# Kernel tuning notes

Measured on AMD Instinct MI355X. Metric: run time of the kernel, lower is better.

## Reference

```python
import jax, jax.numpy as jnp
import numpy as np

B, H = 65536, 512


def setup_inputs() -> dict:
    key = jax.random.key(0)
    ks = jax.random.split(key, 10)
    s = 1.0 / np.sqrt(H)  # torch nn.Linear default init range
    uni = lambda k, shape: jax.random.uniform(k, shape, jnp.float32, -s, s)
    return {
        "inputs": jax.random.normal(ks[0], (B, H), jnp.float32),
        "short_term_memory": jax.random.normal(ks[1], (B, H), jnp.float32),
        "Wf": uni(ks[2], (H, H)), "bf": uni(ks[3], (H,)),
        "Wi": uni(ks[4], (H, H)), "bi": uni(ks[5], (H,)),
        "Wg": uni(ks[6], (H, H)), "bg": uni(ks[7], (H,)),
        "Wo": uni(ks[8], (H, H)), "bo": uni(ks[9], (H,)),
    }


def reference(inputs, short_term_memory, Wf, bf, Wi, bi, Wg, bg, Wo, bo):
    z = inputs + short_term_memory  # [B, H]
    # ForgetGate: OVERWRITES long-term memory (previous cell state never read).
    c = jax.nn.sigmoid(z @ Wf.T + bf)
    # InputGate: c += sigmoid(...) * tanh(...)
    c = c + jax.nn.sigmoid(z @ Wi.T + bi) * jnp.tanh(z @ Wg.T + bg)
    # OutputGate: h = tanh(c) * sigmoid(...)
    h = jnp.tanh(c) * jax.nn.sigmoid(z @ Wo.T + bo)
    return jnp.stack((c, h))  # [2, B, H]: new long-term and short-term memory
```

## Files before the change

### kernel.cpp

```cpp
#include <hip/hip_runtime.h>

typedef __bf16 bf16x8 __attribute__((ext_vector_type(8)));
typedef float  f32x4  __attribute__((ext_vector_type(4)));

#define LOG2E 1.4426950408889634f

static __device__ __forceinline__ float fexp2(float x) { return __builtin_amdgcn_exp2f(x); }
static __device__ __forceinline__ float frcp(float x)  { return __builtin_amdgcn_rcpf(x); }
static __device__ __forceinline__ float fsigmoid(float x) { return frcp(1.0f + fexp2(-LOG2E * x)); }
static __device__ __forceinline__ float ftanh(float x)    { return 2.0f * frcp(1.0f + fexp2(-2.0f * LOG2E * x)) - 1.0f; }

__global__ __launch_bounds__(256) void wpack(const float* __restrict__ Wf,
                                             const float* __restrict__ Wi,
                                             const float* __restrict__ Wg,
                                             const float* __restrict__ Wo,
                                             __bf16* __restrict__ Wp)
{
    int idx = blockIdx.x * 256 + threadIdx.x;
    int kg  = idx & 63;
    int j   = (idx >> 6) & 511;
    int g   = idx >> 15;
    const float* src = (g == 0) ? Wf : (g == 1) ? Wi : (g == 2) ? Wg : Wo;
    const float4* s4 = (const float4*)(src + j * 512 + kg * 8);
    float4 v0 = s4[0], v1 = s4[1];
    bf16x8 o;
    o[0] = (__bf16)v0.x; o[1] = (__bf16)v0.y; o[2] = (__bf16)v0.z; o[3] = (__bf16)v0.w;
    o[4] = (__bf16)v1.x; o[5] = (__bf16)v1.y; o[6] = (__bf16)v1.z; o[7] = (__bf16)v1.w;
    int cn = j >> 4;
    int ks = kg >> 2;
    int lt = (j & 15) + (kg & 3) * 16;
    size_t dst = ((size_t)(((cn * 16 + ks) * 4 + g) * 64 + lt)) * 8;
    *(bf16x8*)(Wp + dst) = o;
}

__global__ __launch_bounds__(512, 2) void lstm_main(
    const float* __restrict__ xin, const float* __restrict__ stm,
    const __bf16* __restrict__ Wp,
    const float* __restrict__ bfv, const float* __restrict__ biv,
    const float* __restrict__ bgv, const float* __restrict__ bov,
    float* __restrict__ out)
{
    __shared__ unsigned char zs[131072];
    const int tid  = threadIdx.x;
    const int lane = tid & 63;
    const int wv   = tid >> 6;
    const int l15  = lane & 15;
    const int lq   = lane >> 4;
    const int row0 = blockIdx.x * 128;

    {
        const float* xb = xin + (size_t)row0 * 512;
        const float* sb = stm + (size_t)row0 * 512;
        #pragma unroll
        for (int it = 0; it < 16; ++it) {
            int idx = it * 512 + tid;
            int row = idx >> 6;
            int kg  = idx & 63;
            const float4* x4 = (const float4*)(xb + row * 512 + kg * 8);
            const float4* s4 = (const float4*)(sb + row * 512 + kg * 8);
            float4 a0 = x4[0], a1 = x4[1];
            float4 b0 = s4[0], b1 = s4[1];
            bf16x8 p;
            p[0] = (__bf16)(a0.x + b0.x); p[1] = (__bf16)(a0.y + b0.y);
            p[2] = (__bf16)(a0.z + b0.z); p[3] = (__bf16)(a0.w + b0.w);
            p[4] = (__bf16)(a1.x + b1.x); p[5] = (__bf16)(a1.y + b1.y);
            p[6] = (__bf16)(a1.z + b1.z); p[7] = (__bf16)(a1.w + b1.w);
            int rb   = row >> 5;
            int kk   = kg >> 1;
            int slot = ((row & 31) + (kg & 1) * 32) ^ (kk & 7);
            *(bf16x8*)(zs + rb * 32768 + kk * 1024 + slot * 16) = p;
        }
    }
    __syncthreads();

    const int kkoff = lq >> 1;
    const int sl0   = l15 + (lq & 1) * 32;
    const int koffb = kkoff << 10;

#define LOADB(B0, B1, B2, B3, KS) { \
    const char* a_ = bp + (KS) * 4096; \
    asm volatile("global_load_dwordx4 %0, %4, off\n\t" \
                 "global_load_dwordx4 %1, %4, off offset:1024\n\t" \
                 "global_load_dwordx4 %2, %4, off offset:2048\n\t" \
                 "global_load_dwordx4 %3, %4, off offset:3072" \
                 : "=&v"(B0), "=&v"(B1), "=&v"(B2), "=&v"(B3) : "v"(a_)); }
#define WAITB4 { asm volatile("s_waitcnt vmcnt(4)"); __builtin_amdgcn_sched_barrier(0x107); }
#define WAITB0 { asm volatile("s_waitcnt vmcnt(0)"); __builtin_amdgcn_sched_barrier(0x107); }
#define DOMFMA(B0, B1, B2, B3, KS) { \
    const int kk7_ = ((2 * (KS)) & 7) | kkoff; \
    const int t0_  = ((sl0 ^ kk7_) << 4) + (KS) * 2048 + koffb; \
    { \
        bf16x8 a0_ = *(const bf16x8*)(zs + t0_); \
        bf16x8 a1_ = *(const bf16x8*)(zs + t0_ + 256); \
        bf16x8 a2_ = *(const bf16x8*)(zs + 32768 + t0_); \
        bf16x8 a3_ = *(const bf16x8*)(zs + 32768 + t0_ + 256); \
        __builtin_amdgcn_s_setprio(1); \
        acc[0][0] = __builtin_amdgcn_mfma_f32_16x16x32_bf16(a0_, B0, acc[0][0], 0, 0, 0); \
        acc[1][0] = __builtin_amdgcn_mfma_f32_16x16x32_bf16(a1_, B0, acc[1][0], 0, 0, 0); \
        acc[2][0] = __builtin_amdgcn_mfma_f32_16x16x32_bf16(a2_, B0, acc[2][0], 0, 0, 0); \
        acc[3][0] = __builtin_amdgcn_mfma_f32_16x16x32_bf16(a3_, B0, acc[3][0], 0, 0, 0); \
        acc[0][1] = __builtin_amdgcn_mfma_f32_16x16x32_bf16(a0_, B1, acc[0][1], 0, 0, 0); \
        acc[1][1] = __builtin_amdgcn_mfma_f32_16x16x32_bf16(a1_, B1, acc[1][1], 0, 0, 0); \
        acc[2][1] = __builtin_amdgcn_mfma_f32_16x16x32_bf16(a2_, B1, acc[2][1], 0, 0, 0); \
        acc[3][1] = __builtin_amdgcn_mfma_f32_16x16x32_bf16(a3_, B1, acc[3][1], 0, 0, 0); \
        acc[0][2] = __builtin_amdgcn_mfma_f32_16x16x32_bf16(a0_, B2, acc[0][2], 0, 0, 0); \
        acc[1][2] = __builtin_amdgcn_mfma_f32_16x16x32_bf16(a1_, B2, acc[1][2], 0, 0, 0); \
        acc[2][2] = __builtin_amdgcn_mfma_f32_16x16x32_bf16(a2_, B2, acc[2][2], 0, 0, 0); \
        acc[3][2] = __builtin_amdgcn_mfma_f32_16x16x32_bf16(a3_, B2, acc[3][2], 0, 0, 0); \
        acc[0][3] = __builtin_amdgcn_mfma_f32_16x16x32_bf16(a0_, B3, acc[0][3], 0, 0, 0); \
        acc[1][3] = __builtin_amdgcn_mfma_f32_16x16x32_bf16(a1_, B3, acc[1][3], 0, 0, 0); \
        acc[2][3] = __builtin_amdgcn_mfma_f32_16x16x32_bf16(a2_, B3, acc[2][3], 0, 0, 0); \
        acc[3][3] = __builtin_amdgcn_mfma_f32_16x16x32_bf16(a3_, B3, acc[3][3], 0, 0, 0); \
        __builtin_amdgcn_s_setprio(0); \
    } \
    { \
        bf16x8 a4_ = *(const bf16x8*)(zs + 65536 + t0_); \
        bf16x8 a5_ = *(const bf16x8*)(zs + 65536 + t0_ + 256); \
        bf16x8 a6_ = *(const bf16x8*)(zs + 98304 + t0_); \
        bf16x8 a7_ = *(const bf16x8*)(zs + 98304 + t0_ + 256); \
        __builtin_amdgcn_s_setprio(1); \
        acc[4][0] = __builtin_amdgcn_mfma_f32_16x16x32_bf16(a4_, B0, acc[4][0], 0, 0, 0); \
        acc[5][0] = __builtin_amdgcn_mfma_f32_16x16x32_bf16(a5_, B0, acc[5][0], 0, 0, 0); \
        acc[6][0] = __builtin_amdgcn_mfma_f32_16x16x32_bf16(a6_, B0, acc[6][0], 0, 0, 0); \
        acc[7][0] = __builtin_amdgcn_mfma_f32_16x16x32_bf16(a7_, B0, acc[7][0], 0, 0, 0); \
        acc[4][1] = __builtin_amdgcn_mfma_f32_16x16x32_bf16(a4_, B1, acc[4][1], 0, 0, 0); \
        acc[5][1] = __builtin_amdgcn_mfma_f32_16x16x32_bf16(a5_, B1, acc[5][1], 0, 0, 0); \
        acc[6][1] = __builtin_amdgcn_mfma_f32_16x16x32_bf16(a6_, B1, acc[6][1], 0, 0, 0); \
        acc[7][1] = __builtin_amdgcn_mfma_f32_16x16x32_bf16(a7_, B1, acc[7][1], 0, 0, 0); \
        acc[4][2] = __builtin_amdgcn_mfma_f32_16x16x32_bf16(a4_, B2, acc[4][2], 0, 0, 0); \
        acc[5][2] = __builtin_amdgcn_mfma_f32_16x16x32_bf16(a5_, B2, acc[5][2], 0, 0, 0); \
        acc[6][2] = __builtin_amdgcn_mfma_f32_16x16x32_bf16(a6_, B2, acc[6][2], 0, 0, 0); \
        acc[7][2] = __builtin_amdgcn_mfma_f32_16x16x32_bf16(a7_, B2, acc[7][2], 0, 0, 0); \
        acc[4][3] = __builtin_amdgcn_mfma_f32_16x16x32_bf16(a4_, B3, acc[4][3], 0, 0, 0); \
        acc[5][3] = __builtin_amdgcn_mfma_f32_16x16x32_bf16(a5_, B3, acc[5][3], 0, 0, 0); \
        acc[6][3] = __builtin_amdgcn_mfma_f32_16x16x32_bf16(a6_, B3, acc[6][3], 0, 0, 0); \
        acc[7][3] = __builtin_amdgcn_mfma_f32_16x16x32_bf16(a7_, B3, acc[7][3], 0, 0, 0); \
        __builtin_amdgcn_s_setprio(0); \
    } }

    for (int ci = 0; ci < 4; ++ci) {
        const int cn   = ci * 8 + wv;
        const int colj = cn * 16 + l15;
        const char* bp = (const char*)Wp + (size_t)cn * 65536 + (size_t)lane * 16;

        float bias0 = bfv[colj], bias1 = biv[colj];
        float bias2 = bgv[colj], bias3 = bov[colj];
        f32x4 acc[8][4];
        #pragma unroll
        for (int m = 0; m < 8; ++m) {
            #pragma unroll
            for (int r = 0; r < 4; ++r) {
                acc[m][0][r] = bias0; acc[m][1][r] = bias1;
                acc[m][2][r] = bias2; acc[m][3][r] = bias3;
            }
        }

        bf16x8 P0, P1, P2, P3;
        bf16x8 Q0, Q1, Q2, Q3;

        asm volatile("s_waitcnt vmcnt(0)");
        __builtin_amdgcn_sched_barrier(0);
        LOADB(P0, P1, P2, P3, 0)
        #pragma unroll
        for (int ks = 0; ks < 16; ++ks) {
            if (ks < 15) {
                if ((ks + 1) & 1) { LOADB(Q0, Q1, Q2, Q3, ks + 1) }
                else              { LOADB(P0, P1, P2, P3, ks + 1) }
                WAITB4
            } else {
                WAITB0
            }
            if (ks & 1) { DOMFMA(Q0, Q1, Q2, Q3, ks) }
            else        { DOMFMA(P0, P1, P2, P3, ks) }
        }

        #pragma unroll
        for (int m = 0; m < 8; ++m) {
            #pragma unroll
            for (int r = 0; r < 4; ++r) {
                float F = acc[m][0][r], I = acc[m][1][r];
                float G = acc[m][2][r], O = acc[m][3][r];
                float c = fsigmoid(F) + fsigmoid(I) * ftanh(G);
                float h = ftanh(c) * fsigmoid(O);
                int row = row0 + m * 16 + lq * 4 + r;
                int o   = row * 512 + colj;
                out[o] = c;
                out[33554432 + o] = h;
            }
        }
    }
#undef LOADB
#undef WAITB4
#undef WAITB0
#undef DOMFMA
}

extern "C" void kernel_launch(void* const* d_in, const int* in_sizes, int n_in,
                              void* d_out, int out_size, void* d_ws, size_t ws_size,
                              hipStream_t stream) {
    const float* xin = (const float*)d_in[0];
    const float* stm = (const float*)d_in[1];
    const float* Wf  = (const float*)d_in[2];
    const float* bf_ = (const float*)d_in[3];
    const float* Wi  = (const float*)d_in[4];
    const float* bi_ = (const float*)d_in[5];
    const float* Wg  = (const float*)d_in[6];
    const float* bg_ = (const float*)d_in[7];
    const float* Wo  = (const float*)d_in[8];
    const float* bo_ = (const float*)d_in[9];
    __bf16* Wp = (__bf16*)d_ws;

    wpack<<<512, 256, 0, stream>>>(Wf, Wi, Wg, Wo, Wp);
    lstm_main<<<512, 512, 0, stream>>>(xin, stm, Wp, bf_, bi_, bg_, bo_, (float*)d_out);
}
```

Before: 183.3 us.

## Overlap staging of z tile into LDS with first column-chunk MFMA loop

Removes the up-front loop that loads inputs and short_term_memory, adds them, converts to bf16 and writes the whole 128-row z tile to LDS before any MFMA work. Instead, the first column chunk streams z one k-slice at a time, with double-buffered global loads and a barrier per slice, interleaved with weight loads and MFMAs. This is meant to hide the activation-load latency behind compute. It adds 16 block barriers in the first chunk and puts more pressure on registers.

```diff
diff --git a/kernel.cpp b/kernel.cpp
--- a/kernel.cpp
+++ b/kernel.cpp
@@ -48,34 +48,17 @@
     const int lq   = lane >> 4;
     const int row0 = blockIdx.x * 128;
 
-    {
-        const float* xb = xin + (size_t)row0 * 512;
-        const float* sb = stm + (size_t)row0 * 512;
-        #pragma unroll
-        for (int it = 0; it < 16; ++it) {
-            int idx = it * 512 + tid;
-            int row = idx >> 6;
-            int kg  = idx & 63;
-            const float4* x4 = (const float4*)(xb + row * 512 + kg * 8);
-            const float4* s4 = (const float4*)(sb + row * 512 + kg * 8);
-            float4 a0 = x4[0], a1 = x4[1];
-            float4 b0 = s4[0], b1 = s4[1];
-            bf16x8 p;
-            p[0] = (__bf16)(a0.x + b0.x); p[1] = (__bf16)(a0.y + b0.y);
-            p[2] = (__bf16)(a0.z + b0.z); p[3] = (__bf16)(a0.w + b0.w);
-            p[4] = (__bf16)(a1.x + b1.x); p[5] = (__bf16)(a1.y + b1.y);
-            p[6] = (__bf16)(a1.z + b1.z); p[7] = (__bf16)(a1.w + b1.w);
-            int rb   = row >> 5;
-            int kk   = kg >> 1;
-            int slot = ((row & 31) + (kg & 1) * 32) ^ (kk & 7);
-            *(bf16x8*)(zs + rb * 32768 + kk * 1024 + slot * 16) = p;
-        }
-    }
-    __syncthreads();
-
     const int kkoff = lq >> 1;
     const int sl0   = l15 + (lq & 1) * 32;
     const int koffb = kkoff << 10;
+
+    const int srow   = tid >> 2;
+    const int kgl    = tid & 3;
+    const int st_kh  = kgl >> 1;
+    const int st_r31 = (srow & 31) + (kgl & 1) * 32;
+    const int st_cb  = (srow >> 5) * 32768;
+    const char* xq = (const char*)xin + ((size_t)(row0 + srow) * 512 + kgl * 8) * 4;
+    const char* sq = (const char*)stm + ((size_t)(row0 + srow) * 512 + kgl * 8) * 4;
 
 #define LOADB(B0, B1, B2, B3, KS) { \
     const char* a_ = bp + (KS) * 4096; \
@@ -84,6 +67,28 @@
                  "global_load_dwordx4 %2, %4, off offset:2048\n\t" \
                  "global_load_dwordx4 %3, %4, off offset:3072" \
                  : "=&v"(B0), "=&v"(B1), "=&v"(B2), "=&v"(B3) : "v"(a_)); }
+#define STLD(X0, X1, S0, S1, J) { \
+    const char* xp_ = xq + (J) * 128; \
+    const char* sp_ = sq + (J) * 128; \
+    asm volatile("global_load_dwordx4 %0, %4, off\n\t" \
+                 "global_load_dwordx4 %1, %4, off offset:16\n\t" \
+                 "global_load_dwordx4 %2, %5, off\n\t" \
+                 "global_load_dwordx4 %3, %5, off offset:16" \
+                 : "=&v"(X0), "=&v"(X1), "=&v"(S0), "=&v"(S1) \
+                 : "v"(xp_), "v"(sp_)); }
+#define STWR(X0, X1, S0, S1, J) { \
+    bf16x8 p_; \
+    p_[0] = (__bf16)(X0[0] + S0[0]); p_[1] = (__bf16)(X0[1] + S0[1]); \
+    p_[2] = (__bf16)(X0[2] + S0[2]); p_[3] = (__bf16)(X0[3] + S0[3]); \
+    p_[4] = (__bf16)(X1[0] + S1[0]); p_[5] = (__bf16)(X1[1] + S1[1]); \
+    p_[6] = (__bf16)(X1[2] + S1[2]); p_[7] = (__bf16)(X1[3] + S1[3]); \
+    const int kk_ = 2 * (J) + st_kh; \
+    *(bf16x8*)(zs + st_cb + kk_ * 1024 + ((st_r31 ^ (kk_ & 7)) << 4)) = p_; \
+    asm volatile("s_waitcnt lgkmcnt(0)" ::: "memory"); \
+    __builtin_amdgcn_s_barrier(); \
+    __builtin_amdgcn_sched_barrier(0); }
+#define WAITC(N) { asm volatile("s_waitcnt vmcnt(" #N ")"); __builtin_amdgcn_sched_barrier(0); }
+#define WAITD(N) { asm volatile("s_waitcnt vmcnt(" #N ")"); __builtin_amdgcn_sched_barrier(0x107); }
 #define WAITB4 { asm volatile("s_waitcnt vmcnt(4)"); __builtin_amdgcn_sched_barrier(0x107); }
 #define WAITB0 { asm volatile("s_waitcnt vmcnt(0)"); __builtin_amdgcn_sched_barrier(0x107); }
 #define DOMFMA(B0, B1, B2, B3, KS) { \
@@ -137,8 +142,91 @@
         acc[7][3] = __builtin_amdgcn_mfma_f32_16x16x32_bf16(a7_, B3, acc[7][3], 0, 0, 0); \
         __builtin_amdgcn_s_setprio(0); \
     } }
-
-    for (int ci = 0; ci < 4; ++ci) {
+#define EPILOG \
+    _Pragma("unroll") \
+    for (int m = 0; m < 8; ++m) { \
+        _Pragma("unroll") \
+        for (int r = 0; r < 4; ++r) { \
+            float F = acc[m][0][r], I = acc[m][1][r]; \
+            float G = acc[m][2][r], O = acc[m][3][r]; \
+            float c = fsigmoid(F) + fsigmoid(I) * ftanh(G); \
+            float h = ftanh(c) * fsigmoid(O); \
+            int row = row0 + m * 16 + lq * 4 + r; \
+            int o   = row * 512 + colj; \
+            out[o] = c; \
+            out[33554432 + o] = h; \
+        } }
+
+    {
+        const int cn   = wv;
+        const int colj = cn * 16 + l15;
+        const char* bp = (const char*)Wp + (size_t)cn * 65536 + (size_t)lane * 16;
+
+        float bias0 = bfv[colj], bias1 = biv[colj];
+        float bias2 = bgv[colj], bias3 = bov[colj];
+        f32x4 acc[8][4];
+        #pragma unroll
+        for (int m = 0; m < 8; ++m) {
+            #pragma unroll
+            for (int r = 0; r < 4; ++r) {
+                acc[m][0][r] = bias0; acc[m][1][r] = bias1;
+                acc[m][2][r] = bias2; acc[m][3][r] = bias3;
+            }
+        }
+
+        f32x4 Ax0, Ax1, As0, As1;
+        f32x4 Bx0, Bx1, Bs0, Bs1;
+        bf16x8 P0, P1, P2, P3;
+        bf16x8 Q0, Q1, Q2, Q3;
+
+        asm volatile("s_waitcnt vmcnt(0)");
+        __builtin_amdgcn_sched_barrier(0);
+        STLD(Ax0, Ax1, As0, As1, 0)
+        STLD(Bx0, Bx1, Bs0, Bs1, 1)
+        LOADB(P0, P1, P2, P3, 0)
+
+#define CSTEP(J, JP1, JP2, N0,N1,N2,N3, C0,C1,C2,C3, SX0,SX1,SS0,SS1) \
+        LOADB(N0, N1, N2, N3, JP1) \
+        WAITC(12) \
+        STWR(SX0, SX1, SS0, SS1, J) \
+        STLD(SX0, SX1, SS0, SS1, JP2) \
+        WAITD(12) \
+        DOMFMA(C0, C1, C2, C3, J)
+
+        LOADB(Q0, Q1, Q2, Q3, 1)
+        WAITC(12)
+        STWR(Ax0, Ax1, As0, As1, 0)
+        STLD(Ax0, Ax1, As0, As1, 2)
+        WAITD(8)
+        DOMFMA(P0, P1, P2, P3, 0)
+        CSTEP( 1,  2,  3, P0,P1,P2,P3, Q0,Q1,Q2,Q3, Bx0,Bx1,Bs0,Bs1)
+        CSTEP( 2,  3,  4, Q0,Q1,Q2,Q3, P0,P1,P2,P3, Ax0,Ax1,As0,As1)
+        CSTEP( 3,  4,  5, P0,P1,P2,P3, Q0,Q1,Q2,Q3, Bx0,Bx1,Bs0,Bs1)
+        CSTEP( 4,  5,  6, Q0,Q1,Q2,Q3, P0,P1,P2,P3, Ax0,Ax1,As0,As1)
+        CSTEP( 5,  6,  7, P0,P1,P2,P3, Q0,Q1,Q2,Q3, Bx0,Bx1,Bs0,Bs1)
+        CSTEP( 6,  7,  8, Q0,Q1,Q2,Q3, P0,P1,P2,P3, Ax0,Ax1,As0,As1)
+        CSTEP( 7,  8,  9, P0,P1,P2,P3, Q0,Q1,Q2,Q3, Bx0,Bx1,Bs0,Bs1)
+        CSTEP( 8,  9, 10, Q0,Q1,Q2,Q3, P0,P1,P2,P3, Ax0,Ax1,As0,As1)
+        CSTEP( 9, 10, 11, P0,P1,P2,P3, Q0,Q1,Q2,Q3, Bx0,Bx1,Bs0,Bs1)
+        CSTEP(10, 11, 12, Q0,Q1,Q2,Q3, P0,P1,P2,P3, Ax0,Ax1,As0,As1)
+        CSTEP(11, 12, 13, P0,P1,P2,P3, Q0,Q1,Q2,Q3, Bx0,Bx1,Bs0,Bs1)
+        CSTEP(12, 13, 14, Q0,Q1,Q2,Q3, P0,P1,P2,P3, Ax0,Ax1,As0,As1)
+        CSTEP(13, 14, 15, P0,P1,P2,P3, Q0,Q1,Q2,Q3, Bx0,Bx1,Bs0,Bs1)
+        LOADB(Q0, Q1, Q2, Q3, 15)
+        WAITC(12)
+        STWR(Ax0, Ax1, As0, As1, 14)
+        WAITD(8)
+        DOMFMA(P0, P1, P2, P3, 14)
+        WAITC(4)
+        STWR(Bx0, Bx1, Bs0, Bs1, 15)
+        WAITD(0)
+        DOMFMA(Q0, Q1, Q2, Q3, 15)
+#undef CSTEP
+
+        EPILOG
+    }
+
+    for (int ci = 1; ci < 4; ++ci) {
         const int cn   = ci * 8 + wv;
         const int colj = cn * 16 + l15;
         const char* bp = (const char*)Wp + (size_t)cn * 65536 + (size_t)lane * 16;
@@ -174,25 +262,17 @@
             else        { DOMFMA(P0, P1, P2, P3, ks) }
         }
 
-        #pragma unroll
-        for (int m = 0; m < 8; ++m) {
-            #pragma unroll
-            for (int r = 0; r < 4; ++r) {
-                float F = acc[m][0][r], I = acc[m][1][r];
-                float G = acc[m][2][r], O = acc[m][3][r];
-                float c = fsigmoid(F) + fsigmoid(I) * ftanh(G);
-                float h = ftanh(c) * fsigmoid(O);
-                int row = row0 + m * 16 + lq * 4 + r;
-                int o   = row * 512 + colj;
-                out[o] = c;
-                out[33554432 + o] = h;
-            }
-        }
+        EPILOG
     }
 #undef LOADB
+#undef STLD
+#undef STWR
+#undef WAITC
+#undef WAITD
 #undef WAITB4
 #undef WAITB0
 #undef DOMFMA
+#undef EPILOG
 }
 
 extern "C" void kernel_launch(void* const* d_in, const int* in_sizes, int n_in,
```

Result: faster. 176.3 us (-3.8%).
